# Optimization experiments

Hardware: AMD Instinct MI355X
Metric: run time of the kernel (lower is better)

The kernel has to match this reference:

```python
import jax, jax.numpy as jnp
import numpy as np


def setup_inputs() -> dict:
    key = jax.random.key(0)
    k1, k2, k3 = jax.random.split(key, 3)
    B, N, D = 64, 1024, 768
    inputs = jax.random.normal(k1, (B, N, D), dtype=jnp.float32)
    x_class = jax.random.normal(k2, (D,), dtype=jnp.float32)
    embeddings = jax.random.normal(k3, (N + 1, D), dtype=jnp.float32)
    return {"inputs": inputs, "x_class": x_class, "embeddings": embeddings}


def reference(inputs, x_class, embeddings):
    # The original tf.while_loop just broadcasts x_class over the batch dim.
    B = inputs.shape[0]
    cls = jnp.broadcast_to(x_class[None, None, :], (B, 1, inputs.shape[2]))  # [B,1,D]
    return jnp.concatenate([cls, inputs], axis=1) + embeddings  # [B,N+1,D]
```

## Files before the change

### kernel.cpp

```cpp
#include <hip/hip_runtime.h>
#include <hip/hip_bf16.h>


#define D4 192
#define NP1 1025

__global__ __launch_bounds__(192)
void pos_embed_kernel(const float4* __restrict__ in4,
                      const float4* __restrict__ cls4,
                      const float4* __restrict__ emb4,
                      float4* __restrict__ out4) {
    const int n  = blockIdx.x;
    const int b  = blockIdx.y;
    const int d4 = threadIdx.x;

    float4 e = emb4[n * D4 + d4];
    float4 s;
    if (n == 0) {
        s = cls4[d4];
    } else {
        s = in4[(b * 1024 + (n - 1)) * D4 + d4];
    }
    float4 r;
    r.x = s.x + e.x;
    r.y = s.y + e.y;
    r.z = s.z + e.z;
    r.w = s.w + e.w;
    out4[(b * NP1 + n) * D4 + d4] = r;
}

extern "C" void kernel_launch(void* const* d_in, const int* in_sizes, int n_in,
                              void* d_out, int out_size, void* d_ws, size_t ws_size,
                              hipStream_t stream) {
    const float4* in4  = (const float4*)d_in[0];
    const float4* cls4 = (const float4*)d_in[1];
    const float4* emb4 = (const float4*)d_in[2];
    float4* out4       = (float4*)d_out;

    dim3 grid(NP1, 64, 1);
    dim3 block(D4, 1, 1);
    pos_embed_kernel<<<grid, block, 0, stream>>>(in4, cls4, emb4, out4);
}
```

Measured before the change: 329.3 us.

## Flatten per-batch bulk add into grid-stride loop with nontemporal loads/stores

Replaces the one-block-per-row launch (1025x64 blocks of 192 threads) with 49x64 blocks of 256 threads. Each block processes 16 float4 elements per thread over the contiguous per-batch bulk region, and a separate block handles the class-token row. Input loads and output stores use nontemporal builtins so the streamed data bypasses cache retention, while the embedding table is read normally so it can stay cached. The aim is lower block scheduling overhead and less cache pollution, at the cost of fewer total waves in flight per launch.

```diff
diff --git a/kernel.cpp b/kernel.cpp
--- a/kernel.cpp
+++ b/kernel.cpp
@@ -2,42 +2,51 @@
 #include <hip/hip_bf16.h>
 
 
-#define D4 192
-#define NP1 1025
+typedef float f4 __attribute__((ext_vector_type(4)));
 
-__global__ __launch_bounds__(192)
-void pos_embed_kernel(const float4* __restrict__ in4,
-                      const float4* __restrict__ cls4,
-                      const float4* __restrict__ emb4,
-                      float4* __restrict__ out4) {
-    const int n  = blockIdx.x;
-    const int b  = blockIdx.y;
-    const int d4 = threadIdx.x;
+#define D4      192
+#define ROWS4   196800
+#define BULK4   196608
+#define BLKS    48
+#define STRIDE  (BLKS * 256)
+#define ITERS   16
 
-    float4 e = emb4[n * D4 + d4];
-    float4 s;
-    if (n == 0) {
-        s = cls4[d4];
-    } else {
-        s = in4[(b * 1024 + (n - 1)) * D4 + d4];
+__global__ __launch_bounds__(256)
+void pos_embed_kernel(const f4* __restrict__ in4,
+                      const f4* __restrict__ cls4,
+                      const f4* __restrict__ emb4,
+                      f4* __restrict__ out4) {
+    const int b = blockIdx.y;
+    const f4* __restrict__ inb  = in4  + (size_t)b * BULK4;
+    f4* __restrict__       outb = out4 + (size_t)b * ROWS4;
+
+    if (blockIdx.x == BLKS) {
+        const int t = threadIdx.x;
+        if (t < D4) {
+            outb[t] = cls4[t] + emb4[t];
+        }
+        return;
     }
-    float4 r;
-    r.x = s.x + e.x;
-    r.y = s.y + e.y;
-    r.z = s.z + e.z;
-    r.w = s.w + e.w;
-    out4[(b * NP1 + n) * D4 + d4] = r;
+
+    int i = blockIdx.x * 256 + threadIdx.x;
+    #pragma unroll
+    for (int k = 0; k < ITERS; ++k, i += STRIDE) {
+        f4 s = __builtin_nontemporal_load(&inb[i]);
+        f4 e = emb4[D4 + i];
+        f4 r = s + e;
+        __builtin_nontemporal_store(r, &outb[D4 + i]);
+    }
 }
 
 extern "C" void kernel_launch(void* const* d_in, const int* in_sizes, int n_in,
                               void* d_out, int out_size, void* d_ws, size_t ws_size,
                               hipStream_t stream) {
-    const float4* in4  = (const float4*)d_in[0];
-    const float4* cls4 = (const float4*)d_in[1];
-    const float4* emb4 = (const float4*)d_in[2];
-    float4* out4       = (float4*)d_out;
+    const f4* in4  = (const f4*)d_in[0];
+    const f4* cls4 = (const f4*)d_in[1];
+    const f4* emb4 = (const f4*)d_in[2];
+    f4* out4       = (f4*)d_out;
 
-    dim3 grid(NP1, 64, 1);
-    dim3 block(D4, 1, 1);
+    dim3 grid(BLKS + 1, 64, 1);
+    dim3 block(256, 1, 1);
     pos_embed_kernel<<<grid, block, 0, stream>>>(in4, cls4, emb4, out4);
 }
```

Result: no change. 328.0 us (-0.4%).
